# Optimization experiments

Hardware: AMD Instinct MI355X
Metric: run time of the kernel (lower is better)

The kernel has to match this reference:

```python
import jax, jax.numpy as jnp
import numpy as np

NUM_GRAPHS = 128
NODES_PER_GRAPH = 512
N_NODES = NUM_GRAPHS * NODES_PER_GRAPH
N_EDGES = 524288
IN_DIM = 128
HID = 128
OUT_DIM = 10
N_LAYERS = 3
POOL_RATIO = 0.5  # TopKPooling default ratio


def setup_inputs() -> dict:
    key = jax.random.key(0)
    ks = jax.random.split(key, 16)
    x = jax.random.normal(ks[0], (N_NODES, IN_DIM), dtype=jnp.float32)
    edge_index = jax.random.randint(ks[1], (2, N_EDGES), 0, N_NODES, dtype=jnp.int64)
    batch = jnp.repeat(jnp.arange(NUM_GRAPHS, dtype=jnp.int64), NODES_PER_GRAPH)
    s = 0.05
    return {
        "x": x,
        "edge_index": edge_index,
        "batch": batch,
        "emb_W": jax.random.normal(ks[2], (IN_DIM, HID), dtype=jnp.float32) * s,
        "emb_b": jnp.zeros((HID,), dtype=jnp.float32),
        "gcn_W": jax.random.normal(ks[3], (N_LAYERS, HID, HID), dtype=jnp.float32) * s,
        "gcn_b": jnp.zeros((N_LAYERS, HID), dtype=jnp.float32),
        "pool_p": jax.random.normal(ks[4], (HID,), dtype=jnp.float32),
        "fc1_W": jax.random.normal(ks[5], (HID, 128), dtype=jnp.float32) * s,
        "fc1_b": jnp.zeros((128,), dtype=jnp.float32),
        "fc2_W": jax.random.normal(ks[6], (128, 64), dtype=jnp.float32) * s,
        "fc2_b": jnp.zeros((64,), dtype=jnp.float32),
        "fc3_W": jax.random.normal(ks[7], (64, OUT_DIM), dtype=jnp.float32) * s,
        "fc3_b": jnp.zeros((OUT_DIM,), dtype=jnp.float32),
    }


def reference(x, edge_index, batch, emb_W, emb_b, gcn_W, gcn_b, pool_p,
              fc1_W, fc1_b, fc2_W, fc2_b, fc3_W, fc3_b):
    n = x.shape[0]
    # embedding
    h = x @ emb_W + emb_b
    # GCNConv normalization (PyG semantics): add self loops, deg from target scatter
    loop = jnp.arange(n, dtype=edge_index.dtype)
    src = jnp.concatenate([edge_index[0], loop])
    dst = jnp.concatenate([edge_index[1], loop])
    deg = jax.ops.segment_sum(jnp.ones_like(src, dtype=h.dtype), dst, num_segments=n)
    dinv = jnp.where(deg > 0, jax.lax.rsqrt(jnp.maximum(deg, 1e-12)), 0.0)
    norm = dinv[src] * dinv[dst]  # [E+n]
    for l in range(gcn_W.shape[0]):
        hw = h @ gcn_W[l]                                   # [n, HID]
        msg = hw[src] * norm[:, None]                        # gather + scale
        h = jax.nn.relu(jax.ops.segment_sum(msg, dst, num_segments=n) + gcn_b[l])
    # TopKPooling (ratio=0.5, tanh nonlinearity), uniform graphs -> reshape + top_k
    npg = n // NUM_GRAPHS
    k = int(np.ceil(POOL_RATIO * npg))
    score = (h @ pool_p) / jnp.linalg.norm(pool_p)           # [n]
    score_g = score.reshape(NUM_GRAPHS, npg)
    topv, topi = jax.lax.top_k(score_g, k)                   # [G, k]
    h_g = h.reshape(NUM_GRAPHS, npg, -1)
    h_sel = jnp.take_along_axis(h_g, topi[:, :, None], axis=1) * jnp.tanh(topv)[:, :, None]
    pooled = h_sel.mean(axis=1)                              # global_mean_pool -> [G, HID]
    # MLP head (dropout is identity in eval)
    z = jax.nn.relu(pooled @ fc1_W + fc1_b)
    z = jax.nn.relu(z @ fc2_W + fc2_b)
    return z @ fc3_W + fc3_b
```

## Files before the change

kernel.cpp:

```cpp
#include <hip/hip_runtime.h>
#include <hip/hip_bf16.h>
#include <math.h>


#define SLOTS 48

static __device__ __forceinline__ float4 f4add(float4 a, float4 b) {
    return make_float4(a.x + b.x, a.y + b.y, a.z + b.z, a.w + b.w);
}
static __device__ __forceinline__ float4 f4fma(float s, float4 a, float4 acc) {
    return make_float4(fmaf(s, a.x, acc.x), fmaf(s, a.y, acc.y),
                       fmaf(s, a.z, acc.z), fmaf(s, a.w, acc.w));
}

__global__ __launch_bounds__(256) void build_graph_fold(
    const int* __restrict__ src, const int* __restrict__ dst,
    int* __restrict__ cnt, int* __restrict__ csr_pad, int E, int EB,
    const float* __restrict__ embW, const float* __restrict__ embb,
    const float* __restrict__ W0, float* __restrict__ W01,
    float* __restrict__ b01)
{
    const int b = blockIdx.x;
    if (b < EB) {
        int e = b * 256 + threadIdx.x;
        if (e < E) {
            int d = dst[e];
            int r = atomicAdd(&cnt[d], 1);
            if (r < SLOTS) csr_pad[d * SLOTS + r] = src[e];
        }
        return;
    }
    __shared__ float rs[128];
    __shared__ float part[256];
    const int r = b - EB;
    const int t = threadIdx.x;
    const int c = t & 127, q = t >> 7;
    if (t < 128) rs[t] = (r < 128) ? embW[r * 128 + t] : embb[t];
    __syncthreads();
    float s = 0.f;
    const int k0 = q * 64;
#pragma unroll 8
    for (int k = k0; k < k0 + 64; k++) s = fmaf(rs[k], W0[k * 128 + c], s);
    part[t] = s;
    __syncthreads();
    if (q == 0) {
        float v = part[c] + part[c + 128];
        if (r < 128) W01[r * 128 + c] = v;
        else         b01[c] = v;
    }
}

#define ASTRIDE 257
#define WSTRIDE 140
__global__ __launch_bounds__(256) void gemm128(
    const float* __restrict__ A, const float* __restrict__ W,
    const float* __restrict__ bias, const int* __restrict__ rowdeg,
    float* __restrict__ out, int n)
{
    __shared__ float As[32 * ASTRIDE];
    __shared__ float Ws[32 * WSTRIDE];
    const int tid  = threadIdx.x;
    const int rb   = blockIdx.x * 128;
    const int tc   = tid & 15;
    const int tr   = tid >> 4;
    const int colg = tc * 8;
    const int cswz = colg + ((colg >> 5) << 2);
    const int rowg = tr * 8;

    const int a_kq = tid & 7;
    const int a_m  = tid >> 3;
    const int w_c  = (tid & 31) * 4;
    const int w_cs = w_c + ((w_c >> 5) << 2);
    const int w_k  = tid >> 5;

    float acc[8][8];
#pragma unroll
    for (int i = 0; i < 8; i++)
#pragma unroll
        for (int j = 0; j < 8; j++) acc[i][j] = 0.f;

    float4 areg[4], wreg[4];
#pragma unroll
    for (int t = 0; t < 4; t++)
        areg[t] = *(const float4*)&A[(size_t)(rb + t * 32 + a_m) * 128 + a_kq * 4];
#pragma unroll
    for (int t = 0; t < 4; t++)
        wreg[t] = *(const float4*)&W[(size_t)(t * 8 + w_k) * 128 + w_c];

#pragma unroll 1
    for (int k0 = 0; k0 < 128; k0 += 32) {
#pragma unroll
        for (int t = 0; t < 4; t++) {
            const int m = t * 32 + a_m;
            const float4 av = areg[t];
            As[(a_kq * 4 + 0) * ASTRIDE + m] = av.x;
            As[(a_kq * 4 + 1) * ASTRIDE + m] = av.y;
            As[(a_kq * 4 + 2) * ASTRIDE + m] = av.z;
            As[(a_kq * 4 + 3) * ASTRIDE + m] = av.w;
        }
#pragma unroll
        for (int t = 0; t < 4; t++)
            *(float4*)&Ws[(t * 8 + w_k) * WSTRIDE + w_cs] = wreg[t];
        __syncthreads();
        if (k0 < 96) {
#pragma unroll
            for (int t = 0; t < 4; t++)
                areg[t] = *(const float4*)&A[(size_t)(rb + t * 32 + a_m) * 128 + k0 + 32 + a_kq * 4];
#pragma unroll
            for (int t = 0; t < 4; t++)
                wreg[t] = *(const float4*)&W[(size_t)(k0 + 32 + t * 8 + w_k) * 128 + w_c];
        }
#pragma unroll 8
        for (int kk = 0; kk < 32; kk++) {
            float4 a0 = *(const float4*)&As[kk * ASTRIDE + rowg];
            float4 a1 = *(const float4*)&As[kk * ASTRIDE + rowg + 4];
            float4 b0 = *(const float4*)&Ws[kk * WSTRIDE + cswz];
            float4 b1 = *(const float4*)&Ws[kk * WSTRIDE + cswz + 4];
            float av[8] = {a0.x, a0.y, a0.z, a0.w, a1.x, a1.y, a1.z, a1.w};
            float bv[8] = {b0.x, b0.y, b0.z, b0.w, b1.x, b1.y, b1.z, b1.w};
#pragma unroll
            for (int i = 0; i < 8; i++)
#pragma unroll
                for (int j = 0; j < 8; j++) acc[i][j] = fmaf(av[i], bv[j], acc[i][j]);
        }
        __syncthreads();
    }

    float4 bb0 = make_float4(0.f, 0.f, 0.f, 0.f), bb1 = bb0;
    if (bias) {
        bb0 = *(const float4*)&bias[colg];
        bb1 = *(const float4*)&bias[colg + 4];
    }
#pragma unroll
    for (int i = 0; i < 8; i++) {
        const int row  = rb + rowg + i;
        const float sc = rowdeg ? rsqrtf((float)(rowdeg[row] + 1)) : 1.f;
        float4 o0, o1;
        o0.x = (acc[i][0] + bb0.x) * sc;  o0.y = (acc[i][1] + bb0.y) * sc;
        o0.z = (acc[i][2] + bb0.z) * sc;  o0.w = (acc[i][3] + bb0.w) * sc;
        o1.x = (acc[i][4] + bb1.x) * sc;  o1.y = (acc[i][5] + bb1.y) * sc;
        o1.z = (acc[i][6] + bb1.z) * sc;  o1.w = (acc[i][7] + bb1.w) * sc;
        *(float4*)&out[(size_t)row * 128 + colg]     = o0;
        *(float4*)&out[(size_t)row * 128 + colg + 4] = o1;
    }
}

__global__ __launch_bounds__(256) void aggregate(
    const float* __restrict__ hs, const int* __restrict__ csr_pad,
    const int* __restrict__ cnt, const float* __restrict__ bias,
    float* __restrict__ hout,
    const float* __restrict__ pool_p, float* __restrict__ scores, int n)
{
    const int grp  = threadIdx.x >> 5;
    const int lane = threadIdx.x & 31;
    const int node = blockIdx.x * 8 + grp;
    const float4* __restrict__ hv = (const float4*)hs;

    const int deg = cnt[node];
    const int e0  = node * SLOTS;

    int   ix[16];
    float mk[16];
#pragma unroll
    for (int j = 0; j < 16; j++) {
        const int raw = csr_pad[e0 + j];
        const bool v  = j < deg;
        ix[j] = v ? raw : node;
        mk[j] = v ? 1.f : 0.f;
    }

    float4 self = hv[(size_t)node * 32 + lane];
    float4 r[16];
#pragma unroll
    for (int j = 0; j < 16; j++)
        r[j] = hv[(size_t)ix[j] * 32 + lane];
    asm volatile("" ::: "memory");

    float4 a0 = self;
    float4 a1 = make_float4(0.f, 0.f, 0.f, 0.f);
    float4 a2 = a1, a3 = a1;
#pragma unroll
    for (int j = 0; j < 16; j += 4) {
        a0 = f4fma(mk[j + 0], r[j + 0], a0);
        a1 = f4fma(mk[j + 1], r[j + 1], a1);
        a2 = f4fma(mk[j + 2], r[j + 2], a2);
        a3 = f4fma(mk[j + 3], r[j + 3], a3);
    }
    const int dcap = deg < SLOTS ? deg : SLOTS;
    for (int j = 16; j < dcap; j++) {
        a1 = f4add(a1, hv[(size_t)csr_pad[e0 + j] * 32 + lane]);
    }

    float4 s = f4add(f4add(a0, a1), f4add(a2, a3));
    const float dv = rsqrtf((float)(deg + 1));
    const float4 bb = ((const float4*)bias)[lane];
    float4 o;
    o.x = fmaxf(fmaf(s.x, dv, bb.x), 0.f);
    o.y = fmaxf(fmaf(s.y, dv, bb.y), 0.f);
    o.z = fmaxf(fmaf(s.z, dv, bb.z), 0.f);
    o.w = fmaxf(fmaf(s.w, dv, bb.w), 0.f);
    ((float4*)hout)[(size_t)node * 32 + lane] = o;

    if (scores) {
        float4 pv = ((const float4*)pool_p)[lane];
        float d  = o.x * pv.x + o.y * pv.y + o.z * pv.z + o.w * pv.w;
        float nn = pv.x * pv.x + pv.y * pv.y + pv.z * pv.z + pv.w * pv.w;
#pragma unroll
        for (int off = 16; off > 0; off >>= 1) {
            d  += __shfl_xor(d, off);
            nn += __shfl_xor(nn, off);
        }
        if (lane == 0) scores[node] = d * rsqrtf(nn);
    }
}

__global__ __launch_bounds__(512) void topk_mlp(
    const float* __restrict__ scores, const float* __restrict__ h,
    const float* __restrict__ fc1W, const float* __restrict__ fc1b,
    const float* __restrict__ fc2W, const float* __restrict__ fc2b,
    const float* __restrict__ fc3W, const float* __restrict__ fc3b,
    float* __restrict__ out)
{
    __shared__ float s[512];
    __shared__ int   sel[256];
    __shared__ float w[256];
    __shared__ float4 red[512];
    __shared__ float pld[128];
    __shared__ float z1[128];
    __shared__ float z2[64];
    const int g = blockIdx.x;
    const int i = threadIdx.x;
    s[i] = scores[g * 512 + i];
    __syncthreads();
    float si = s[i];
    int rank = 0;
    for (int j = 0; j < 512; j++) {
        float sj = s[j];
        rank += (sj > si) || (sj == si && j < i);
    }
    if (rank < 256) {
        sel[rank] = i;
        w[rank]   = tanhf(si) * (1.f / 256.f);
    }
    __syncthreads();
    const int c   = (i & 31) * 4;
    const int grp = i >> 5;
    float4 acc = make_float4(0.f, 0.f, 0.f, 0.f);
    for (int t = grp; t < 256; t += 16) {
        float wt  = w[t];
        int   idx = sel[t];
        float4 r = *(const float4*)&h[((size_t)g * 512 + idx) * 128 + c];
        acc = f4fma(wt, r, acc);
    }
    red[i] = acc;
    __syncthreads();
    if (i < 256) red[i] = f4add(red[i], red[i + 256]);
    __syncthreads();
    if (i < 128) red[i] = f4add(red[i], red[i + 128]);
    __syncthreads();
    if (i < 64) red[i] = f4add(red[i], red[i + 64]);
    __syncthreads();
    if (i < 32) {
        float4 v = f4add(red[i], red[i + 32]);
        *(float4*)&pld[i * 4] = v;
    }
    __syncthreads();
    if (i < 128) {
        float a = fc1b[i];
        for (int k = 0; k < 128; k++) a += pld[k] * fc1W[k * 128 + i];
        z1[i] = fmaxf(a, 0.f);
    }
    __syncthreads();
    if (i < 64) {
        float b = fc2b[i];
        for (int k = 0; k < 128; k++) b += z1[k] * fc2W[k * 64 + i];
        z2[i] = fmaxf(b, 0.f);
    }
    __syncthreads();
    if (i < 10) {
        float o = fc3b[i];
        for (int k = 0; k < 64; k++) o += z2[k] * fc3W[k * 10 + i];
        out[g * 10 + i] = o;
    }
}

extern "C" void kernel_launch(void* const* d_in, const int* in_sizes, int n_in,
                              void* d_out, int out_size, void* d_ws, size_t ws_size,
                              hipStream_t stream)
{
    const float* x     = (const float*)d_in[0];
    const int*   eidx  = (const int*)d_in[1];
    const float* embW  = (const float*)d_in[3];
    const float* embb  = (const float*)d_in[4];
    const float* gcnW  = (const float*)d_in[5];
    const float* gcnb  = (const float*)d_in[6];
    const float* poolp = (const float*)d_in[7];
    const float* fc1W  = (const float*)d_in[8];
    const float* fc1b  = (const float*)d_in[9];
    const float* fc2W  = (const float*)d_in[10];
    const float* fc2b  = (const float*)d_in[11];
    const float* fc3W  = (const float*)d_in[12];
    const float* fc3b  = (const float*)d_in[13];
    float* out = (float*)d_out;

    const int n = in_sizes[0] / 128;
    const int E = in_sizes[1] / 2;
    const int G = n / 512;

    const int* src = eidx;
    const int* dst = eidx + E;

    char* ws = (char*)d_ws;
    size_t off = 0;
    auto carve = [&](size_t bytes) {
        void* p = ws + off;
        off += (bytes + 255) & ~(size_t)255;
        return p;
    };
    float* h       = (float*)carve((size_t)n * 128 * 4);
    float* hs      = (float*)carve((size_t)n * 128 * 4);
    int*   cnt     = (int*)carve((size_t)n * 4);
    int*   csr_pad = (int*)carve((size_t)n * SLOTS * 4);
    float* scores  = (float*)carve((size_t)n * 4);
    float* W01     = (float*)carve(128 * 128 * 4);
    float* b01     = (float*)carve(128 * 4);
    (void)ws_size;

    const int EB = E / 256;

    hipMemsetAsync(cnt, 0, (size_t)n * 4, stream);
    build_graph_fold<<<EB + 129, 256, 0, stream>>>(
        src, dst, cnt, csr_pad, E, EB, embW, embb, gcnW, W01, b01);

    gemm128<<<n / 128, 256, 0, stream>>>(x, W01, b01, cnt, hs, n);
    aggregate<<<n / 8, 256, 0, stream>>>(hs, csr_pad, cnt, gcnb, h,
                                         poolp, nullptr, n);

    for (int l = 1; l < 3; l++) {
        gemm128<<<n / 128, 256, 0, stream>>>(h, gcnW + (size_t)l * 128 * 128,
                                             nullptr, cnt, hs, n);
        aggregate<<<n / 8, 256, 0, stream>>>(
            hs, csr_pad, cnt, gcnb + (size_t)l * 128, h,
            poolp, (l == 2) ? scores : nullptr, n);
    }

    topk_mlp<<<G, 512, 0, stream>>>(scores, h, fc1W, fc1b, fc2W, fc2b,
                                    fc3W, fc3b, out);
}
```

Measured before the change: 392.8 us.

## Overlap CSR build with first GEMM and move source-degree scaling into aggregation

The edge-bucketing work moves out of the weight-fold kernel and into extra blocks of the first GEMM launch, so graph construction runs alongside the first layer's matmul rather than ahead of it. Because degrees are no longer final when that GEMM runs, the per-row source normalization comes out of the GEMM epilogue. The aggregation kernel now applies it per neighbor by reading cnt of each neighbor, and its unrolled gather depth drops from 16 to 12. The top-k/MLP kernel is widened to 1024 threads to halve the pooling gather loop, at the cost of an extra reduction step and extra random cnt reads during aggregation.

```diff
diff --git a/kernel.cpp b/kernel.cpp
--- a/kernel.cpp
+++ b/kernel.cpp
@@ -4,6 +4,7 @@
 
 
 #define SLOTS 48
+#define FLAT  12
 
 static __device__ __forceinline__ float4 f4add(float4 a, float4 b) {
     return make_float4(a.x + b.x, a.y + b.y, a.z + b.z, a.w + b.w);
@@ -13,26 +14,14 @@
                        fmaf(s, a.z, acc.z), fmaf(s, a.w, acc.w));
 }
 
-__global__ __launch_bounds__(256) void build_graph_fold(
-    const int* __restrict__ src, const int* __restrict__ dst,
-    int* __restrict__ cnt, int* __restrict__ csr_pad, int E, int EB,
+__global__ __launch_bounds__(256) void fold_emb(
     const float* __restrict__ embW, const float* __restrict__ embb,
     const float* __restrict__ W0, float* __restrict__ W01,
     float* __restrict__ b01)
 {
-    const int b = blockIdx.x;
-    if (b < EB) {
-        int e = b * 256 + threadIdx.x;
-        if (e < E) {
-            int d = dst[e];
-            int r = atomicAdd(&cnt[d], 1);
-            if (r < SLOTS) csr_pad[d * SLOTS + r] = src[e];
-        }
-        return;
-    }
     __shared__ float rs[128];
     __shared__ float part[256];
-    const int r = b - EB;
+    const int r = blockIdx.x;
     const int t = threadIdx.x;
     const int c = t & 127, q = t >> 7;
     if (t < 128) rs[t] = (r < 128) ? embW[r * 128 + t] : embb[t];
@@ -54,13 +43,25 @@
 #define WSTRIDE 140
 __global__ __launch_bounds__(256) void gemm128(
     const float* __restrict__ A, const float* __restrict__ W,
-    const float* __restrict__ bias, const int* __restrict__ rowdeg,
-    float* __restrict__ out, int n)
-{
+    const float* __restrict__ bias, float* __restrict__ out,
+    const int* __restrict__ src, const int* __restrict__ dst,
+    int* __restrict__ cnt, int* __restrict__ csr_pad, int E, int gb)
+{
+    const int bid = blockIdx.x;
+    if (bid >= gb) {
+        int e = (bid - gb) * 256 + threadIdx.x;
+        if (e < E) {
+            int d = dst[e];
+            int r = atomicAdd(&cnt[d], 1);
+            if (r < SLOTS) csr_pad[d * SLOTS + r] = src[e];
+        }
+        return;
+    }
+
     __shared__ float As[32 * ASTRIDE];
     __shared__ float Ws[32 * WSTRIDE];
     const int tid  = threadIdx.x;
-    const int rb   = blockIdx.x * 128;
+    const int rb   = bid * 128;
     const int tc   = tid & 15;
     const int tr   = tid >> 4;
     const int colg = tc * 8;
@@ -133,13 +134,12 @@
     }
 #pragma unroll
     for (int i = 0; i < 8; i++) {
-        const int row  = rb + rowg + i;
-        const float sc = rowdeg ? rsqrtf((float)(rowdeg[row] + 1)) : 1.f;
+        const int row = rb + rowg + i;
         float4 o0, o1;
-        o0.x = (acc[i][0] + bb0.x) * sc;  o0.y = (acc[i][1] + bb0.y) * sc;
-        o0.z = (acc[i][2] + bb0.z) * sc;  o0.w = (acc[i][3] + bb0.w) * sc;
-        o1.x = (acc[i][4] + bb1.x) * sc;  o1.y = (acc[i][5] + bb1.y) * sc;
-        o1.z = (acc[i][6] + bb1.z) * sc;  o1.w = (acc[i][7] + bb1.w) * sc;
+        o0.x = acc[i][0] + bb0.x;  o0.y = acc[i][1] + bb0.y;
+        o0.z = acc[i][2] + bb0.z;  o0.w = acc[i][3] + bb0.w;
+        o1.x = acc[i][4] + bb1.x;  o1.y = acc[i][5] + bb1.y;
+        o1.z = acc[i][6] + bb1.z;  o1.w = acc[i][7] + bb1.w;
         *(float4*)&out[(size_t)row * 128 + colg]     = o0;
         *(float4*)&out[(size_t)row * 128 + colg + 4] = o1;
     }
@@ -159,40 +159,42 @@
     const int deg = cnt[node];
     const int e0  = node * SLOTS;
 
-    int   ix[16];
-    float mk[16];
-#pragma unroll
-    for (int j = 0; j < 16; j++) {
+    int   ix[FLAT];
+    float dj[FLAT];
+#pragma unroll
+    for (int j = 0; j < FLAT; j++) {
         const int raw = csr_pad[e0 + j];
-        const bool v  = j < deg;
-        ix[j] = v ? raw : node;
-        mk[j] = v ? 1.f : 0.f;
-    }
-
+        ix[j] = (j < deg) ? raw : node;
+    }
+#pragma unroll
+    for (int j = 0; j < FLAT; j++)
+        dj[j] = (j < deg) ? rsqrtf((float)(cnt[ix[j]] + 1)) : 0.f;
+
+    const float dv = rsqrtf((float)(deg + 1));
     float4 self = hv[(size_t)node * 32 + lane];
-    float4 r[16];
-#pragma unroll
-    for (int j = 0; j < 16; j++)
+    float4 r[FLAT];
+#pragma unroll
+    for (int j = 0; j < FLAT; j++)
         r[j] = hv[(size_t)ix[j] * 32 + lane];
     asm volatile("" ::: "memory");
 
-    float4 a0 = self;
+    float4 a0 = make_float4(self.x * dv, self.y * dv, self.z * dv, self.w * dv);
     float4 a1 = make_float4(0.f, 0.f, 0.f, 0.f);
     float4 a2 = a1, a3 = a1;
 #pragma unroll
-    for (int j = 0; j < 16; j += 4) {
-        a0 = f4fma(mk[j + 0], r[j + 0], a0);
-        a1 = f4fma(mk[j + 1], r[j + 1], a1);
-        a2 = f4fma(mk[j + 2], r[j + 2], a2);
-        a3 = f4fma(mk[j + 3], r[j + 3], a3);
+    for (int j = 0; j < FLAT; j += 4) {
+        a0 = f4fma(dj[j + 0], r[j + 0], a0);
+        a1 = f4fma(dj[j + 1], r[j + 1], a1);
+        a2 = f4fma(dj[j + 2], r[j + 2], a2);
+        a3 = f4fma(dj[j + 3], r[j + 3], a3);
     }
     const int dcap = deg < SLOTS ? deg : SLOTS;
-    for (int j = 16; j < dcap; j++) {
-        a1 = f4add(a1, hv[(size_t)csr_pad[e0 + j] * 32 + lane]);
+    for (int j = FLAT; j < dcap; j++) {
+        const int idx = csr_pad[e0 + j];
+        a1 = f4fma(rsqrtf((float)(cnt[idx] + 1)), hv[(size_t)idx * 32 + lane], a1);
     }
 
     float4 s = f4add(f4add(a0, a1), f4add(a2, a3));
-    const float dv = rsqrtf((float)(deg + 1));
     const float4 bb = ((const float4*)bias)[lane];
     float4 o;
     o.x = fmaxf(fmaf(s.x, dv, bb.x), 0.f);
@@ -214,7 +216,7 @@
     }
 }
 
-__global__ __launch_bounds__(512) void topk_mlp(
+__global__ __launch_bounds__(1024) void topk_mlp(
     const float* __restrict__ scores, const float* __restrict__ h,
     const float* __restrict__ fc1W, const float* __restrict__ fc1b,
     const float* __restrict__ fc2W, const float* __restrict__ fc2b,
@@ -224,35 +226,39 @@
     __shared__ float s[512];
     __shared__ int   sel[256];
     __shared__ float w[256];
-    __shared__ float4 red[512];
+    __shared__ float4 red[1024];
     __shared__ float pld[128];
     __shared__ float z1[128];
     __shared__ float z2[64];
     const int g = blockIdx.x;
     const int i = threadIdx.x;
-    s[i] = scores[g * 512 + i];
-    __syncthreads();
-    float si = s[i];
-    int rank = 0;
-    for (int j = 0; j < 512; j++) {
-        float sj = s[j];
-        rank += (sj > si) || (sj == si && j < i);
-    }
-    if (rank < 256) {
-        sel[rank] = i;
-        w[rank]   = tanhf(si) * (1.f / 256.f);
+    if (i < 512) s[i] = scores[g * 512 + i];
+    __syncthreads();
+    if (i < 512) {
+        float si = s[i];
+        int rank = 0;
+        for (int j = 0; j < 512; j++) {
+            float sj = s[j];
+            rank += (sj > si) || (sj == si && j < i);
+        }
+        if (rank < 256) {
+            sel[rank] = i;
+            w[rank]   = tanhf(si) * (1.f / 256.f);
+        }
     }
     __syncthreads();
     const int c   = (i & 31) * 4;
     const int grp = i >> 5;
     float4 acc = make_float4(0.f, 0.f, 0.f, 0.f);
-    for (int t = grp; t < 256; t += 16) {
+    for (int t = grp; t < 256; t += 32) {
         float wt  = w[t];
         int   idx = sel[t];
         float4 r = *(const float4*)&h[((size_t)g * 512 + idx) * 128 + c];
         acc = f4fma(wt, r, acc);
     }
     red[i] = acc;
+    __syncthreads();
+    if (i < 512) red[i] = f4add(red[i], red[i + 512]);
     __syncthreads();
     if (i < 256) red[i] = f4add(red[i], red[i + 256]);
     __syncthreads();
@@ -326,24 +332,23 @@
     float* b01     = (float*)carve(128 * 4);
     (void)ws_size;
 
+    const int gb = n / 128;
     const int EB = E / 256;
 
     hipMemsetAsync(cnt, 0, (size_t)n * 4, stream);
-    build_graph_fold<<<EB + 129, 256, 0, stream>>>(
-        src, dst, cnt, csr_pad, E, EB, embW, embb, gcnW, W01, b01);
-
-    gemm128<<<n / 128, 256, 0, stream>>>(x, W01, b01, cnt, hs, n);
+    fold_emb<<<129, 256, 0, stream>>>(embW, embb, gcnW, W01, b01);
+    gemm128<<<gb + EB, 256, 0, stream>>>(x, W01, b01, hs,
+                                         src, dst, cnt, csr_pad, E, gb);
     aggregate<<<n / 8, 256, 0, stream>>>(hs, csr_pad, cnt, gcnb, h,
                                          poolp, nullptr, n);
-
     for (int l = 1; l < 3; l++) {
-        gemm128<<<n / 128, 256, 0, stream>>>(h, gcnW + (size_t)l * 128 * 128,
-                                             nullptr, cnt, hs, n);
+        gemm128<<<gb, 256, 0, stream>>>(h, gcnW + (size_t)l * 128 * 128,
+                                        nullptr, hs,
+                                        nullptr, nullptr, nullptr, nullptr, 0, gb);
         aggregate<<<n / 8, 256, 0, stream>>>(
             hs, csr_pad, cnt, gcnb + (size_t)l * 128, h,
             poolp, (l == 2) ? scores : nullptr, n);
     }
-
-    topk_mlp<<<G, 512, 0, stream>>>(scores, h, fc1W, fc1b, fc2W, fc2b,
-                                    fc3W, fc3b, out);
-}
+    topk_mlp<<<G, 1024, 0, stream>>>(scores, h, fc1W, fc1b, fc2W, fc2b,
+                                     fc3W, fc3b, out);
+}
```

Result: slower. 412.1 us (+4.9%).

## Fuse all stages into one persistent cooperative kernel with grid syncs

Applied to the files above, without the earlier changes.

Replaces the separate graph build, GEMM, aggregation and top-k/MLP launches with a single cooperative kernel. Blocks loop over tiles or node groups, and grid.sync() separates the phases. The memset is also folded in, and top-k now runs with 256 threads per graph. This removes launch gaps and inter-kernel bubbles. The risk is that the large static shared-memory buffer, shared by every phase, limits resident blocks and hurts latency hiding in the gather-heavy aggregation.

```diff
diff --git a/kernel.cpp b/kernel.cpp
--- a/kernel.cpp
+++ b/kernel.cpp
@@ -1,9 +1,16 @@
 #include <hip/hip_runtime.h>
+#include <hip/hip_cooperative_groups.h>
 #include <hip/hip_bf16.h>
 #include <math.h>
 
+namespace cg = cooperative_groups;
+
 
 #define SLOTS 48
+#define FLAT  16
+#define ASTRIDE 257
+#define WSTRIDE 140
+#define SMEM_FLOATS (32 * ASTRIDE + 32 * WSTRIDE)
 
 static __device__ __forceinline__ float4 f4add(float4 a, float4 b) {
     return make_float4(a.x + b.x, a.y + b.y, a.z + b.z, a.w + b.w);
@@ -13,26 +20,14 @@
                        fmaf(s, a.z, acc.z), fmaf(s, a.w, acc.w));
 }
 
-__global__ __launch_bounds__(256) void build_graph_fold(
-    const int* __restrict__ src, const int* __restrict__ dst,
-    int* __restrict__ cnt, int* __restrict__ csr_pad, int E, int EB,
-    const float* __restrict__ embW, const float* __restrict__ embb,
-    const float* __restrict__ W0, float* __restrict__ W01,
-    float* __restrict__ b01)
-{
-    const int b = blockIdx.x;
-    if (b < EB) {
-        int e = b * 256 + threadIdx.x;
-        if (e < E) {
-            int d = dst[e];
-            int r = atomicAdd(&cnt[d], 1);
-            if (r < SLOTS) csr_pad[d * SLOTS + r] = src[e];
-        }
-        return;
-    }
-    __shared__ float rs[128];
-    __shared__ float part[256];
-    const int r = b - EB;
+static __device__ void fold_row(int r, const float* __restrict__ embW,
+                                const float* __restrict__ embb,
+                                const float* __restrict__ W0,
+                                float* __restrict__ W01, float* __restrict__ b01,
+                                float* smem)
+{
+    float* rs   = smem;
+    float* part = smem + 128;
     const int t = threadIdx.x;
     const int c = t & 127, q = t >> 7;
     if (t < 128) rs[t] = (r < 128) ? embW[r * 128 + t] : embb[t];
@@ -48,19 +43,19 @@
         if (r < 128) W01[r * 128 + c] = v;
         else         b01[c] = v;
     }
-}
-
-#define ASTRIDE 257
-#define WSTRIDE 140
-__global__ __launch_bounds__(256) void gemm128(
-    const float* __restrict__ A, const float* __restrict__ W,
-    const float* __restrict__ bias, const int* __restrict__ rowdeg,
-    float* __restrict__ out, int n)
-{
-    __shared__ float As[32 * ASTRIDE];
-    __shared__ float Ws[32 * WSTRIDE];
+    __syncthreads();
+}
+
+static __device__ void gemm_tile(const float* __restrict__ A,
+                                 const float* __restrict__ W,
+                                 const float* __restrict__ bias,
+                                 const int* __restrict__ cnt,
+                                 float* __restrict__ out, int tile, float* smem)
+{
+    float* As = smem;
+    float* Ws = smem + 32 * ASTRIDE;
     const int tid  = threadIdx.x;
-    const int rb   = blockIdx.x * 128;
+    const int rb   = tile * 128;
     const int tc   = tid & 15;
     const int tr   = tid >> 4;
     const int colg = tc * 8;
@@ -134,7 +129,7 @@
 #pragma unroll
     for (int i = 0; i < 8; i++) {
         const int row  = rb + rowg + i;
-        const float sc = rowdeg ? rsqrtf((float)(rowdeg[row] + 1)) : 1.f;
+        const float sc = rsqrtf((float)(cnt[row] + 1));
         float4 o0, o1;
         o0.x = (acc[i][0] + bb0.x) * sc;  o0.y = (acc[i][1] + bb0.y) * sc;
         o0.z = (acc[i][2] + bb0.z) * sc;  o0.w = (acc[i][3] + bb0.w) * sc;
@@ -145,24 +140,26 @@
     }
 }
 
-__global__ __launch_bounds__(256) void aggregate(
-    const float* __restrict__ hs, const int* __restrict__ csr_pad,
-    const int* __restrict__ cnt, const float* __restrict__ bias,
-    float* __restrict__ hout,
-    const float* __restrict__ pool_p, float* __restrict__ scores, int n)
+static __device__ void agg_group(const float* __restrict__ hs,
+                                 const int* __restrict__ csr_pad,
+                                 const int* __restrict__ cnt,
+                                 const float* __restrict__ bias,
+                                 float* __restrict__ hout,
+                                 const float* __restrict__ pool_p,
+                                 float* __restrict__ scores, int gg)
 {
     const int grp  = threadIdx.x >> 5;
     const int lane = threadIdx.x & 31;
-    const int node = blockIdx.x * 8 + grp;
+    const int node = gg * 8 + grp;
     const float4* __restrict__ hv = (const float4*)hs;
 
     const int deg = cnt[node];
     const int e0  = node * SLOTS;
 
-    int   ix[16];
-    float mk[16];
-#pragma unroll
-    for (int j = 0; j < 16; j++) {
+    int   ix[FLAT];
+    float mk[FLAT];
+#pragma unroll
+    for (int j = 0; j < FLAT; j++) {
         const int raw = csr_pad[e0 + j];
         const bool v  = j < deg;
         ix[j] = v ? raw : node;
@@ -170,9 +167,9 @@
     }
 
     float4 self = hv[(size_t)node * 32 + lane];
-    float4 r[16];
-#pragma unroll
-    for (int j = 0; j < 16; j++)
+    float4 r[FLAT];
+#pragma unroll
+    for (int j = 0; j < FLAT; j++)
         r[j] = hv[(size_t)ix[j] * 32 + lane];
     asm volatile("" ::: "memory");
 
@@ -180,14 +177,14 @@
     float4 a1 = make_float4(0.f, 0.f, 0.f, 0.f);
     float4 a2 = a1, a3 = a1;
 #pragma unroll
-    for (int j = 0; j < 16; j += 4) {
+    for (int j = 0; j < FLAT; j += 4) {
         a0 = f4fma(mk[j + 0], r[j + 0], a0);
         a1 = f4fma(mk[j + 1], r[j + 1], a1);
         a2 = f4fma(mk[j + 2], r[j + 2], a2);
         a3 = f4fma(mk[j + 3], r[j + 3], a3);
     }
     const int dcap = deg < SLOTS ? deg : SLOTS;
-    for (int j = 16; j < dcap; j++) {
+    for (int j = FLAT; j < dcap; j++) {
         a1 = f4add(a1, hv[(size_t)csr_pad[e0 + j] * 32 + lane]);
     }
 
@@ -214,47 +211,50 @@
     }
 }
 
-__global__ __launch_bounds__(512) void topk_mlp(
-    const float* __restrict__ scores, const float* __restrict__ h,
-    const float* __restrict__ fc1W, const float* __restrict__ fc1b,
-    const float* __restrict__ fc2W, const float* __restrict__ fc2b,
-    const float* __restrict__ fc3W, const float* __restrict__ fc3b,
-    float* __restrict__ out)
-{
-    __shared__ float s[512];
-    __shared__ int   sel[256];
-    __shared__ float w[256];
-    __shared__ float4 red[512];
-    __shared__ float pld[128];
-    __shared__ float z1[128];
-    __shared__ float z2[64];
-    const int g = blockIdx.x;
+static __device__ void topk_mlp_graph(int g, const float* __restrict__ scores,
+                                      const float* __restrict__ h,
+                                      const float* __restrict__ fc1W,
+                                      const float* __restrict__ fc1b,
+                                      const float* __restrict__ fc2W,
+                                      const float* __restrict__ fc2b,
+                                      const float* __restrict__ fc3W,
+                                      const float* __restrict__ fc3b,
+                                      float* __restrict__ out, float* smem)
+{
+    float*  s   = smem;
+    float*  w   = smem + 512;
+    float*  pld = smem + 768;
+    float*  z1  = smem + 896;
+    float*  z2  = smem + 1024;
+    int*    sel = (int*)(smem + 1088);
+    float4* red = (float4*)(smem + 1344);
     const int i = threadIdx.x;
-    s[i] = scores[g * 512 + i];
-    __syncthreads();
-    float si = s[i];
-    int rank = 0;
-    for (int j = 0; j < 512; j++) {
-        float sj = s[j];
-        rank += (sj > si) || (sj == si && j < i);
-    }
-    if (rank < 256) {
-        sel[rank] = i;
-        w[rank]   = tanhf(si) * (1.f / 256.f);
+
+    s[i]       = scores[g * 512 + i];
+    s[i + 256] = scores[g * 512 + 256 + i];
+    __syncthreads();
+#pragma unroll
+    for (int half = 0; half < 2; half++) {
+        const int idx = i + half * 256;
+        const float si = s[idx];
+        int rank = 0;
+        for (int j = 0; j < 512; j++) {
+            float sj = s[j];
+            rank += (sj > si) || (sj == si && j < idx);
+        }
+        if (rank < 256) {
+            sel[rank] = idx;
+            w[rank]   = tanhf(si) * (1.f / 256.f);
+        }
     }
     __syncthreads();
     const int c   = (i & 31) * 4;
     const int grp = i >> 5;
     float4 acc = make_float4(0.f, 0.f, 0.f, 0.f);
-    for (int t = grp; t < 256; t += 16) {
-        float wt  = w[t];
-        int   idx = sel[t];
-        float4 r = *(const float4*)&h[((size_t)g * 512 + idx) * 128 + c];
-        acc = f4fma(wt, r, acc);
+    for (int t = grp; t < 256; t += 8) {
+        acc = f4fma(w[t], *(const float4*)&h[((size_t)g * 512 + sel[t]) * 128 + c], acc);
     }
     red[i] = acc;
-    __syncthreads();
-    if (i < 256) red[i] = f4add(red[i], red[i + 256]);
     __syncthreads();
     if (i < 128) red[i] = f4add(red[i], red[i + 128]);
     __syncthreads();
@@ -282,6 +282,68 @@
         for (int k = 0; k < 64; k++) o += z2[k] * fc3W[k * 10 + i];
         out[g * 10 + i] = o;
     }
+    __syncthreads();
+}
+
+__global__ __launch_bounds__(256) void fused_all(
+    const float* __restrict__ x, const int* __restrict__ src,
+    const int* __restrict__ dst,
+    const float* __restrict__ embW, const float* __restrict__ embb,
+    const float* __restrict__ gcnW, const float* __restrict__ gcnb,
+    const float* __restrict__ poolp,
+    const float* __restrict__ fc1W, const float* __restrict__ fc1b,
+    const float* __restrict__ fc2W, const float* __restrict__ fc2b,
+    const float* __restrict__ fc3W, const float* __restrict__ fc3b,
+    float* __restrict__ out,
+    float* __restrict__ h, float* __restrict__ hs,
+    int* __restrict__ cnt, int* __restrict__ csr_pad,
+    float* __restrict__ scores,
+    float* __restrict__ W01, float* __restrict__ b01,
+    int n, int E)
+{
+    cg::grid_group grid = cg::this_grid();
+    __shared__ float smem[SMEM_FLOATS];
+    const int nb  = gridDim.x;
+    const int bid = blockIdx.x;
+    const int tid = threadIdx.x;
+    const int nt  = nb * 256;
+
+    for (int i = bid * 256 + tid; i < n; i += nt) cnt[i] = 0;
+    grid.sync();
+
+    for (int e = bid * 256 + tid; e < E; e += nt) {
+        int d = dst[e];
+        int r = atomicAdd(&cnt[d], 1);
+        if (r < SLOTS) csr_pad[d * SLOTS + r] = src[e];
+    }
+    if (bid < 129)
+        fold_row(bid, embW, embb, gcnW, W01, b01, smem);
+    grid.sync();
+
+    const int tiles  = n / 128;
+    const int groups = n / 8;
+
+    for (int t = bid; t < tiles; t += nb) gemm_tile(x, W01, b01, cnt, hs, t, smem);
+    grid.sync();
+    for (int g = bid; g < groups; g += nb)
+        agg_group(hs, csr_pad, cnt, gcnb, h, poolp, nullptr, g);
+    grid.sync();
+    for (int t = bid; t < tiles; t += nb)
+        gemm_tile(h, gcnW + 128 * 128, nullptr, cnt, hs, t, smem);
+    grid.sync();
+    for (int g = bid; g < groups; g += nb)
+        agg_group(hs, csr_pad, cnt, gcnb + 128, h, poolp, nullptr, g);
+    grid.sync();
+    for (int t = bid; t < tiles; t += nb)
+        gemm_tile(h, gcnW + 2 * 128 * 128, nullptr, cnt, hs, t, smem);
+    grid.sync();
+    for (int g = bid; g < groups; g += nb)
+        agg_group(hs, csr_pad, cnt, gcnb + 256, h, poolp, scores, g);
+    grid.sync();
+
+    for (int g = bid; g < n / 512; g += nb)
+        topk_mlp_graph(g, scores, h, fc1W, fc1b, fc2W, fc2b, fc3W, fc3b,
+                       out, smem);
 }
 
 extern "C" void kernel_launch(void* const* d_in, const int* in_sizes, int n_in,
@@ -305,7 +367,6 @@
 
     const int n = in_sizes[0] / 128;
     const int E = in_sizes[1] / 2;
-    const int G = n / 512;
 
     const int* src = eidx;
     const int* dst = eidx + E;
@@ -326,24 +387,21 @@
     float* b01     = (float*)carve(128 * 4);
     (void)ws_size;
 
-    const int EB = E / 256;
-
-    hipMemsetAsync(cnt, 0, (size_t)n * 4, stream);
-    build_graph_fold<<<EB + 129, 256, 0, stream>>>(
-        src, dst, cnt, csr_pad, E, EB, embW, embb, gcnW, W01, b01);
-
-    gemm128<<<n / 128, 256, 0, stream>>>(x, W01, b01, cnt, hs, n);
-    aggregate<<<n / 8, 256, 0, stream>>>(hs, csr_pad, cnt, gcnb, h,
-                                         poolp, nullptr, n);
-
-    for (int l = 1; l < 3; l++) {
-        gemm128<<<n / 128, 256, 0, stream>>>(h, gcnW + (size_t)l * 128 * 128,
-                                             nullptr, cnt, hs, n);
-        aggregate<<<n / 8, 256, 0, stream>>>(
-            hs, csr_pad, cnt, gcnb + (size_t)l * 128, h,
-            poolp, (l == 2) ? scores : nullptr, n);
-    }
-
-    topk_mlp<<<G, 512, 0, stream>>>(scores, h, fc1W, fc1b, fc2W, fc2b,
-                                    fc3W, fc3b, out);
-}
+    int maxb = 0;
+    hipOccupancyMaxActiveBlocksPerMultiprocessor(&maxb, fused_all, 256, 0);
+    if (maxb < 1) maxb = 1;
+    int grid = maxb * 256;
+    if (grid < 256) grid = 256;
+
+    void* args[] = {
+        (void*)&x, (void*)&src, (void*)&dst,
+        (void*)&embW, (void*)&embb, (void*)&gcnW, (void*)&gcnb,
+        (void*)&poolp, (void*)&fc1W, (void*)&fc1b,
+        (void*)&fc2W, (void*)&fc2b, (void*)&fc3W, (void*)&fc3b,
+        (void*)&out, (void*)&h, (void*)&hs,
+        (void*)&cnt, (void*)&csr_pad, (void*)&scores,
+        (void*)&W01, (void*)&b01, (void*)&n, (void*)&E
+    };
+    hipLaunchCooperativeKernel((const void*)fused_all, dim3(grid), dim3(256),
+                               args, 0, stream);
+}
```

After: 806.1 us. +105.2%, slower.
